# Kernel optimization log

Hardware: AMD Instinct MI355X
Metric: run time of the kernel (lower is better)

Reference implementation:

```python
import jax, jax.numpy as jnp
import numpy as np
from jax import lax

B, L = 32, 1024
N_NODES, FEAT = 100000, 512
DM, DI, DS, DCONV, DTR = 512, 1024, 16, 4, 32  # d_model, d_inner=2*dm, d_state, d_conv, dt_rank=ceil(dm/16)
NL = 2
NCLS = 40
EPS_RMS = 1e-8


def setup_inputs() -> dict:
    key = jax.random.key(0)
    ks = jax.random.split(key, 20)
    s = 0.02
    inp = {
        'sequence': jax.random.randint(ks[0], (B, L), 0, N_NODES),
        'inclusion': (jax.random.uniform(ks[1], (B, L)) < 0.5).astype(jnp.float32),
        'embeddings': jax.random.normal(ks[2], (N_NODES, FEAT), jnp.float32),
        'fc1_w': jax.random.normal(ks[3], (DM, FEAT), jnp.float32) * s,
        'fc1_b': jnp.zeros((DM,), jnp.float32),
        'fc2_w': jax.random.normal(ks[4], (NCLS, DM), jnp.float32) * s,
        'fc2_b': jnp.zeros((NCLS,), jnp.float32),
        'norm_scale': jnp.ones((NL, DM), jnp.float32),
        'in_proj_w': jax.random.normal(ks[5], (NL, 2 * DI, DM), jnp.float32) * s,
        'conv_w': jax.random.normal(ks[6], (NL, DI, 1, DCONV), jnp.float32) * s,
        'conv_b': jnp.zeros((NL, DI), jnp.float32),
        'x_proj_w': jax.random.normal(ks[7], (NL, DTR + 2 * DS, DI), jnp.float32) * s,
        'dt_proj_w': jax.random.normal(ks[8], (NL, DI, DTR), jnp.float32) * s,
        'dt_proj_b': jax.random.uniform(ks[9], (NL, DI), jnp.float32, -4.0, -2.0),
        'A_log': jnp.broadcast_to(jnp.log(jnp.arange(1, DS + 1, dtype=jnp.float32)), (NL, DI, DS)).copy(),
        'D': jnp.ones((NL, DI), jnp.float32),
    }
    return inp


def _rmsnorm(x, scale):
    # x / (||x||_2 / sqrt(d) + eps) * scale  (matches torch RMSNorm with p<0)
    rms = jnp.linalg.norm(x, axis=-1, keepdims=True) * (x.shape[-1] ** -0.5)
    return scale * (x / (rms + EPS_RMS))


def _mamba_block(x, ipw, cw, cb, xpw, dpw, dpb, A_log, Dp):
    # x: (B, L, DM)
    xz = jnp.einsum('bld,ed->ble', x, ipw)              # (B,L,2*DI)
    xin, z = jnp.split(xz, 2, axis=-1)                   # each (B,L,DI)
    # depthwise causal conv1d
    xc = lax.conv_general_dilated(
        xin.transpose(0, 2, 1), cw, (1,), [(DCONV - 1, 0)],
        dimension_numbers=('NCH', 'OIH', 'NCH'), feature_group_count=DI)
    xin = jax.nn.silu((xc + cb[None, :, None]).transpose(0, 2, 1))  # (B,L,DI)
    x_dbl = jnp.einsum('bld,ed->ble', xin, xpw)          # (B,L,DTR+2*DS)
    dt, Bm, Cm = jnp.split(x_dbl, [DTR, DTR + DS], axis=-1)
    delta = jax.nn.softplus(jnp.einsum('blr,dr->bld', dt, dpw) + dpb)  # (B,L,DI)
    A = -jnp.exp(A_log)                                   # (DI,DS)

    def step(h, inp):
        d_t, B_t, C_t, x_t = inp                         # (B,DI),(B,DS),(B,DS),(B,DI)
        dA = jnp.exp(d_t[..., None] * A)                 # (B,DI,DS)
        h = h * dA + (d_t * x_t)[..., None] * B_t[:, None, :]
        y = jnp.einsum('bds,bs->bd', h, C_t)
        return h, y

    h0 = jnp.zeros((x.shape[0], DI, DS), x.dtype)
    xs = (delta.transpose(1, 0, 2), Bm.transpose(1, 0, 2), Cm.transpose(1, 0, 2), xin.transpose(1, 0, 2))
    _, ys = lax.scan(step, h0, xs)                        # (L,B,DI)
    y = ys.transpose(1, 0, 2) + Dp * xin                  # (B,L,DI)
    y = y * jax.nn.silu(z)
    return jnp.einsum('bld,ed->ble', y, jnp.swapaxes(jnp.zeros((0,)), 0, 0) if False else None) if False else y  # placeholder removed below


def _mamba(x, ipw, cw, cb, xpw, dpw, dpb, A_log, Dp, opw):
    y = _mamba_block(x, ipw, cw, cb, xpw, dpw, dpb, A_log, Dp)
    return jnp.einsum('bld,ed->ble', y, opw)


def reference(sequence, inclusion, embeddings, fc1_w, fc1_b, fc2_w, fc2_b,
              norm_scale, in_proj_w, conv_w, conv_b, x_proj_w, dt_proj_w,
              dt_proj_b, A_log, D, out_proj_w=None):
    emb = embeddings @ fc1_w.T + fc1_b                    # (N, DM)
    subg = emb[sequence]                                  # (B, L, DM)
    for i in range(NL):
        zi = _rmsnorm(subg, norm_scale[i])                # prenorm
        # mamba block with out_proj folded: out_proj_w defaults below
        opw = out_proj_w[i] if out_proj_w is not None else jnp.eye(DM, DI, dtype=subg.dtype) * 0.0
        y = _mamba_block(zi, in_proj_w[i], conv_w[i], conv_b[i], x_proj_w[i],
                         dt_proj_w[i], dt_proj_b[i], A_log[i], D[i])
        # out projection (DI -> DM): derive from in_proj slice if no out_proj given
        zi = jnp.einsum('bld,ed->ble', y, in_proj_w[i][:DM, :].T @ jnp.eye(DM, dtype=subg.dtype)) if out_proj_w is None else jnp.einsum('bld,ed->ble', y, opw)
        subg = subg + zi                                  # residual (dropout is identity in eval)
    emb_seq = emb[sequence]
    mask = inclusion[..., None]                           # (B,L,1)
    pooled = jnp.sum(subg * mask, axis=1) / (jnp.sum(mask, axis=1) + 1e-5)
    return pooled @ fc2_w.T + fc2_b


# --- cleaner final version: include explicit out_proj weights ---

def setup_inputs() -> dict:  # noqa: F811 (final definition)
    key = jax.random.key(0)
    ks = jax.random.split(key, 20)
    s = 0.02
    return {
        'sequence': jax.random.randint(ks[0], (B, L), 0, N_NODES),
        'inclusion': (jax.random.uniform(ks[1], (B, L)) < 0.5).astype(jnp.float32),
        'embeddings': jax.random.normal(ks[2], (N_NODES, FEAT), jnp.float32),
        'fc1_w': jax.random.normal(ks[3], (DM, FEAT), jnp.float32) * s,
        'fc1_b': jnp.zeros((DM,), jnp.float32),
        'fc2_w': jax.random.normal(ks[4], (NCLS, DM), jnp.float32) * s,
        'fc2_b': jnp.zeros((NCLS,), jnp.float32),
        'norm_scale': jnp.ones((NL, DM), jnp.float32),
        'in_proj_w': jax.random.normal(ks[5], (NL, 2 * DI, DM), jnp.float32) * s,
        'conv_w': jax.random.normal(ks[6], (NL, DI, 1, DCONV), jnp.float32) * s,
        'conv_b': jnp.zeros((NL, DI), jnp.float32),
        'x_proj_w': jax.random.normal(ks[7], (NL, DTR + 2 * DS, DI), jnp.float32) * s,
        'dt_proj_w': jax.random.normal(ks[8], (NL, DI, DTR), jnp.float32) * s,
        'dt_proj_b': jax.random.uniform(ks[9], (NL, DI), jnp.float32, -4.0, -2.0),
        'A_log': jnp.broadcast_to(jnp.log(jnp.arange(1, DS + 1, dtype=jnp.float32)), (NL, DI, DS)).copy(),
        'D': jnp.ones((NL, DI), jnp.float32),
        'out_proj_w': jax.random.normal(ks[10], (NL, DM, DI), jnp.float32) * s,
    }


def reference(sequence, inclusion, embeddings, fc1_w, fc1_b, fc2_w, fc2_b,
              norm_scale, in_proj_w, conv_w, conv_b, x_proj_w, dt_proj_w,
              dt_proj_b, A_log, D, out_proj_w):  # noqa: F811 (final definition)
    emb = embeddings @ fc1_w.T + fc1_b                    # (N, DM)
    subg = emb[sequence]                                  # (B, L, DM)
    for i in range(NL):
        zi = _rmsnorm(subg, norm_scale[i])                # prenorm RMSNorm
        zi = _mamba(zi, in_proj_w[i], conv_w[i], conv_b[i], x_proj_w[i],
                    dt_proj_w[i], dt_proj_b[i], A_log[i], D[i], out_proj_w[i])
        subg = subg + zi                                  # residual; dropout identity (eval)
    mask = inclusion[..., None]                           # (B,L,1)
    pooled = jnp.sum(subg * mask, axis=1) / (jnp.sum(mask, axis=1) + 1e-5)
    return pooled @ fc2_w.T + fc2_b
```

## Files before the change

kernel.cpp:

```cpp
#include <hip/hip_runtime.h>
#include <cstdint>
#include <cstddef>

#define LSEQ   1024
#define BATCH  32
#define NFEAT  512
#define DMODEL 512
#define DINNER 1024
#define DSTATE 16
#define DTRANK 32
#define NCLASS 40
#define MROWS  (BATCH * LSEQ)
#define NCHUNK 16
#define CLEN   (LSEQ / NCHUNK)

typedef unsigned short u16;
typedef __attribute__((ext_vector_type(8))) __bf16 bf16x8;
typedef __attribute__((ext_vector_type(4))) float f32x4;
typedef __attribute__((ext_vector_type(8))) unsigned short u16x8;

__device__ __forceinline__ u16 f2bf(float x) {
    union { float f; unsigned u; } v; v.f = x;
    unsigned r = v.u + 0x7fffu + ((v.u >> 16) & 1u);
    return (u16)(r >> 16);
// ... 63 lines not shown

    const int cb0 = ((quad)     ^ (frow & 7)) * 8;
    const int cb1 = ((4 + quad) ^ (frow & 7)) * 8;

#define STAGE_A(sb, tt, q) GLL16(gA + (size_t)(q) * 64 * lda + (size_t)(tt) * 64, \
                                 &As[sb][(q) * 4096 + tid * 8])
#define STAGE_B(sb, tt, q) GLL16(gB + (size_t)(q) * 64 * ldb + (size_t)(tt) * 64, \
                                 &Bs[sb][(q) * 4096 + tid * 8])

    f32x4 acc[8][4];
#pragma unroll
    for (int i = 0; i < 8; ++i)
#pragma unroll
        for (int j = 0; j < 4; ++j) acc[i][j] = (f32x4){0.f, 0.f, 0.f, 0.f};

    const int NT = K >> 6;

#pragma unroll
    for (int q = 0; q < 4; ++q) STAGE_A(0, 0, q);
#pragma unroll
    for (int q = 0; q < 4; ++q) STAGE_B(0, 0, q);
#pragma unroll
    for (int q = 0; q < 4; ++q) STAGE_A(1, 1, q);
#pragma unroll
    for (int q = 0; q < 4; ++q) STAGE_B(1, 1, q);
    asm volatile("s_waitcnt vmcnt(8)" ::: "memory");
    __builtin_amdgcn_s_barrier();

    for (int t = 0; t < NT; ++t) {
        const int bsel = t & 1;
        const u16* __restrict__ Ab = &As[bsel][0];
        const u16* __restrict__ Bb = &Bs[bsel][0];
        const int stage = (t + 2 < NT);
        const int t2 = t + 2;
        const int rA = wr + frow;
        const int rB = wc + frow;
        bf16x8 af[4][2], b0[2][2], b1[2][2];

#pragma unroll
        for (int m = 0; m < 4; ++m) {
            const u16* p = Ab + (rA + m * 16) * 64;
            af[m][0] = *(const bf16x8*)(p + cb0);
            af[m][1] = *(const bf16x8*)(p + cb1);
        }
#pragma unroll
        for (int n = 0; n < 2; ++n) {
            const u16* p = Bb + (rB + n * 16) * 64;
            b0[n][0] = *(const bf16x8*)(p + cb0);
            b0[n][1] = *(const bf16x8*)(p + cb1);
        }
        if (stage) { STAGE_A(bsel, t2, 0); STAGE_A(bsel, t2, 2); }
        __builtin_amdgcn_s_barrier();
        asm volatile("s_waitcnt lgkmcnt(0)" ::: "memory");
        __builtin_amdgcn_sched_barrier(0);
        __builtin_amdgcn_s_setprio(1);
#pragma unroll
        for (int m = 0; m < 4; ++m)
#pragma unroll
            for (int n = 0; n < 2; ++n) {
                acc[m][n] = __builtin_amdgcn_mfma_f32_16x16x32_bf16(af[m][0], b0[n][0], acc[m][n], 0, 0, 0);
                acc[m][n] = __builtin_amdgcn_mfma_f32_16x16x32_bf16(af[m][1], b0[n][1], acc[m][n], 0, 0, 0);
            }
        __builtin_amdgcn_s_setprio(0);
        __builtin_amdgcn_s_barrier();

#pragma unroll
        for (int n = 0; n < 2; ++n) {
            const u16* p = Bb + (rB + 32 + n * 16) * 64;
            b1[n][0] = *(const bf16x8*)(p + cb0);
            b1[n][1] = *(const bf16x8*)(p + cb1);
        }
        if (stage) { STAGE_B(bsel, t2, 0); STAGE_B(bsel, t2, 1); }
        __builtin_amdgcn_s_barrier();
        asm volatile("s_waitcnt lgkmcnt(0)" ::: "memory");
        __builtin_amdgcn_sched_barrier(0);
        __builtin_amdgcn_s_setprio(1);
#pragma unroll
        for (int m = 0; m < 4; ++m)
#pragma unroll
            for (int n = 0; n < 2; ++n) {
                acc[m][2 + n] = __builtin_amdgcn_mfma_f32_16x16x32_bf16(af[m][0], b1[n][0], acc[m][2 + n], 0, 0, 0);
                acc[m][2 + n] = __builtin_amdgcn_mfma_f32_16x16x32_bf16(af[m][1], b1[n][1], acc[m][2 + n], 0, 0, 0);
            }
        __builtin_amdgcn_s_setprio(0);
        __builtin_amdgcn_s_barrier();

#pragma unroll
        for (int m = 0; m < 4; ++m) {
            const u16* p = Ab + (rA + 64 + m * 16) * 64;
            af[m][0] = *(const bf16x8*)(p + cb0);
            af[m][1] = *(const bf16x8*)(p + cb1);
        }
        if (stage) { STAGE_A(bsel, t2, 1); STAGE_A(bsel, t2, 3); }
        __builtin_amdgcn_s_barrier();
        asm volatile("s_waitcnt lgkmcnt(0)" ::: "memory");
        __builtin_amdgcn_sched_barrier(0);
        __builtin_amdgcn_s_setprio(1);
#pragma unroll
        for (int m = 0; m < 4; ++m)
#pragma unroll
            for (int n = 0; n < 2; ++n) {
                acc[4 + m][2 + n] = __builtin_amdgcn_mfma_f32_16x16x32_bf16(af[m][0], b1[n][0], acc[4 + m][2 + n], 0, 0, 0);
                acc[4 + m][2 + n] = __builtin_amdgcn_mfma_f32_16x16x32_bf16(af[m][1], b1[n][1], acc[4 + m][2 + n], 0, 0, 0);
            }
        __builtin_amdgcn_s_setprio(0);
        __builtin_amdgcn_s_barrier();

        if (stage) {
            STAGE_B(bsel, t2, 2); STAGE_B(bsel, t2, 3);
            asm volatile("s_waitcnt vmcnt(8)" ::: "memory");
        } else {
            asm volatile("s_waitcnt vmcnt(0)" ::: "memory");
        }
        __builtin_amdgcn_s_barrier();
        __builtin_amdgcn_s_setprio(1);
#pragma unroll
        for (int m = 0; m < 4; ++m)
#pragma unroll
            for (int n = 0; n < 2; ++n) {
                acc[4 + m][n] = __builtin_amdgcn_mfma_f32_16x16x32_bf16(af[m][0], b0[n][0], acc[4 + m][n], 0, 0, 0);
                acc[4 + m][n] = __builtin_amdgcn_mfma_f32_16x16x32_bf16(af[m][1], b0[n][1], acc[4 + m][n], 0, 0, 0);
            }
        __builtin_amdgcn_s_setprio(0);
        __builtin_amdgcn_s_barrier();
    }
#undef STAGE_A
#undef STAGE_B

    float bv[4];
#pragma unroll
    for (int n = 0; n < 4; ++n) {
        int col = n0 + wc + (n >> 1) * 32 + (n & 1) * 16 + frow;
        bv[n] = bias ? bias[col] : 0.f;
    }
#pragma unroll
    for (int m = 0; m < 8; ++m) {
        size_t row0 = (size_t)(m0 + wr + (m >> 2) * 64 + (m & 3) * 16 + quad * 4);
#pragma unroll
        for (int r = 0; r < 4; ++r) {
#pragma unroll
            for (int n = 0; n < 4; ++n) {
                int col = n0 + wc + (n >> 1) * 32 + (n & 1) * 16 + frow;
                size_t cidx = (row0 + r) * (size_t)ldc + (size_t)col;
                float v = acc[m][n][r] + bv[n];
                if (col >= silu_from) v = silu_hw(v);
                if (OUT_BF16)      ((u16*)Cv)[cidx] = f2bf(v);
                else if (ACCUM)    ((float*)Cv)[cidx] += v;
                else               ((float*)Cv)[cidx] = v;
            }
        }
    }
}

template<int OUT_BF16, int ACCUM, int ACT>
__global__ __launch_bounds__(256) void gemm_bt(
    const u16* __restrict__ A, int lda,
    const u16* __restrict__ B, int ldb,
    void* __restrict__ Cv, int ldc,
    const float* __restrict__ bias, int K)
{
    __shared__ __align__(16) u16 As[128 * 32];
    __shared__ __align__(16) u16 Bs[128 * 32];
    const int tid  = threadIdx.x;
    const int m0   = blockIdx.x * 128;
    const int n0   = blockIdx.y * 128;
    const int r0   = tid >> 2;
    const int c0   = (tid & 3) << 3;
    const int lane = tid & 63;
    const int wave = tid >> 6;
    const int wr   = (wave >> 1) << 6;
    const int wc   = (wave & 1) << 6;
    const int frow = lane & 15;
    const int fk   = (lane >> 4) << 3;
    const int quad = lane >> 4;

    const u16* Ap0 = A + (size_t)(m0 + r0) * lda + c0;
    const u16* Ap1 = Ap0 + (size_t)64 * lda;
    const u16* Bp0 = B + (size_t)(n0 + r0) * ldb + c0;
    const u16* Bp1 = Bp0 + (size_t)64 * ldb;
    u16* lA0 = As + tid * 8;  u16* lA1 = As + (tid + 256) * 8;
    u16* lB0 = Bs + tid * 8;  u16* lB1 = Bs + (tid + 256) * 8;

    f32x4 acc[4][4];
#pragma unroll
    for (int i = 0; i < 4; ++i)
#pragma unroll
        for (int j = 0; j < 4; ++j) acc[i][j] = (f32x4){0.f, 0.f, 0.f, 0.f};

    for (int k0 = 0; k0 < K; k0 += 32) {
        GLL16(Ap0 + k0, lA0);
        GLL16(Ap1 + k0, lA1);
        GLL16(Bp0 + k0, lB0);
        GLL16(Bp1 + k0, lB1);
        __syncthreads();
        bf16x8 af[4], bfr[4];
#pragma unroll
        for (int i = 0; i < 4; ++i) {
            af[i]  = *(const bf16x8*)(As + (wr + i * 16 + frow) * 32 + fk);
            bfr[i] = *(const bf16x8*)(Bs + (wc + i * 16 + frow) * 32 + fk);
        }
#pragma unroll
        for (int i = 0; i < 4; ++i)
#pragma unroll
            for (int j = 0; j < 4; ++j)
                acc[i][j] = __builtin_amdgcn_mfma_f32_16x16x32_bf16(
                    af[i], bfr[j], acc[i][j], 0, 0, 0);
        __syncthreads();
    }

    float bv[4];
#pragma unroll
    for (int j = 0; j < 4; ++j)
        bv[j] = bias ? bias[n0 + wc + j * 16 + frow] : 0.f;

#pragma unroll
    for (int i = 0; i < 4; ++i) {
#pragma unroll
        for (int r = 0; r < 4; ++r) {
            size_t row = (size_t)(m0 + wr + i * 16 + quad * 4 + r);
#pragma unroll
            for (int j = 0; j < 4; ++j) {
                size_t cidx = row * (size_t)ldc + (size_t)(n0 + wc + j * 16 + frow);
                float v = acc[i][j][r] + bv[j];
                if (ACT == 1) v = softplus_hw(v);
                if (OUT_BF16)      ((u16*)Cv)[cidx] = f2bf(v);
                else if (ACCUM)    ((float*)Cv)[cidx] += v;
                else               ((float*)Cv)[cidx] = v;
            }
        }
    }
}


#define CVT_N_FC1 65536
#define CVT_N_IP  524288
#define CVT_N_OP  262144
#define CVT_N_DT  16384
#define CVT_TOTAL (CVT_N_FC1 + CVT_N_IP + CVT_N_OP + CVT_N_DT)

__global__ __launch_bounds__(256) void prep_weights_kernel(
    const float* __restrict__ fc1w, u16* __restrict__ wfc1,
    const float* __restrict__ ipw,  u16* __restrict__ wip,
    const float* __restrict__ opw,  u16* __restrict__ wop,
    const float* __restrict__ dtw,  u16* __restrict__ wdt)
{
    int i = blockIdx.x * 256 + threadIdx.x;
    if (i >= CVT_TOTAL) return;
    const float* src; u16* dst; int j = i;
    if (j < CVT_N_FC1)                    { src = fc1w; dst = wfc1; }
    else if ((j -= CVT_N_FC1) < CVT_N_IP) { src = ipw;  dst = wip;  }
    else if ((j -= CVT_N_IP) < CVT_N_OP)  { src = opw;  dst = wop;  }
    else { j -= CVT_N_OP;                   src = dtw;  dst = wdt;  }
    float4 v = ((const float4*)src)[j];
    ushort4 o; o.x = f2bf(v.x); o.y = f2bf(v.y); o.z = f2bf(v.z); o.w = f2bf(v.w);
    ((ushort4*)dst)[j] = o;
}

__global__ __launch_bounds__(256) void pad_xpw_kernel(
    const float* __restrict__ src, u16* __restrict__ dst)
{
    int i  = blockIdx.x * 256 + threadIdx.x;
    int k4 = i & 255;
    int r  = (i >> 8) & 127;
    int l  = i >> 15;
    ushort4 o;
    if (r < 64) {
        float4 v = ((const float4*)(src + ((size_t)l * 64 + r) * DINNER))[k4];
        o.x = f2bf(v.x); o.y = f2bf(v.y); o.z = f2bf(v.z); o.w = f2bf(v.w);
    } else { o.x = 0; o.y = 0; o.z = 0; o.w = 0; }
    ((ushort4*)dst)[i] = o;
}

__global__ __launch_bounds__(256) void gather_kernel(
    const int* __restrict__ seq, const float* __restrict__ emb, u16* __restrict__ g)
{
    int i   = blockIdx.x * 256 + threadIdx.x;
    int row = i >> 7, c = i & 127;
    int node = seq[row];
    float4 v = ((const float4*)(emb + (size_t)node * NFEAT))[c];
    ushort4 o; o.x = f2bf(v.x); o.y = f2bf(v.y); o.z = f2bf(v.z); o.w = f2bf(v.w);
    ((ushort4*)g)[i] = o;
}

__global__ __launch_bounds__(256) void rmsnorm_kernel(
    const float* __restrict__ x, const float* __restrict__ scale, u16* __restrict__ o)
{
    int wave = threadIdx.x >> 6, lane = threadIdx.x & 63;
    size_t row = (size_t)blockIdx.x * 4 + wave;
    const float4* xr = (const float4*)(x + row * DMODEL);
    float4 v0 = xr[lane], v1 = xr[lane + 64];
    float ss = v0.x*v0.x + v0.y*v0.y + v0.z*v0.z + v0.w*v0.w
             + v1.x*v1.x + v1.y*v1.y + v1.z*v1.z + v1.w*v1.w;
#pragma unroll
    for (int off = 32; off; off >>= 1) ss += __shfl_xor(ss, off, 64);
    float inv = 1.f / (sqrtf(ss * (1.f / DMODEL)) + 1e-8f);
    const float4* sc = (const float4*)scale;
    float4 s0 = sc[lane], s1 = sc[lane + 64];
    ushort4 o0, o1;
    o0.x = f2bf(v0.x * s0.x * inv); o0.y = f2bf(v0.y * s0.y * inv);
    o0.z = f2bf(v0.z * s0.z * inv); o0.w = f2bf(v0.w * s0.w * inv);
    o1.x = f2bf(v1.x * s1.x * inv); o1.y = f2bf(v1.y * s1.y * inv);
    o1.z = f2bf(v1.z * s1.z * inv); o1.w = f2bf(v1.w * s1.w * inv);
    ushort4* op = (ushort4*)(o + row * DMODEL);
    op[lane] = o0; op[lane + 64] = o1;
}

__global__ __launch_bounds__(256) void conv_silu_kernel(
    const u16* __restrict__ xz,
    const float* __restrict__ w, const float* __restrict__ cbv,
    u16* __restrict__ xc)
{
    int i  = blockIdx.x * 256 + threadIdx.x;
    int d0 = (i & 127) << 3;
    int r  = i >> 7;
    int l  = r & (LSEQ - 1);
    const u16* bx = xz + (size_t)r * (2 * DINNER) + d0;
    u16x8 zero{};
    u16x8 t3 = *(const u16x8*)(bx);
    u16x8 t2 = (l >= 1) ? *(const u16x8*)(bx - 2 * DINNER) : zero;
    u16x8 t1 = (l >= 2) ? *(const u16x8*)(bx - 4 * DINNER) : zero;
    u16x8 t0 = (l >= 3) ? *(const u16x8*)(bx - 6 * DINNER) : zero;
    u16x8 oc;
#pragma unroll
    for (int c = 0; c < 8; ++c) {
        float4 wc = ((const float4*)w)[d0 + c];
        float acc = cbv[d0 + c]
                  + wc.x * bf2f(t0[c]) + wc.y * bf2f(t1[c])
                  + wc.z * bf2f(t2[c]) + wc.w * bf2f(t3[c]);
        oc[c] = f2bf(silu_hw(acc));
    }
    *(u16x8*)(xc + (size_t)r * DINNER + d0) = oc;
}

__device__ __forceinline__ int detect_s4d(const float* a2) {
    int fast = 1;
#pragma unroll
    for (int s = 1; s < DSTATE; ++s)
        fast &= (__builtin_fabsf(a2[s] - (float)(s + 1) * a2[0]) <=
                 1e-4f * (float)(s + 1) * __builtin_fabsf(a2[0]) + 1e-6f);
    return fast;
}

__global__ __launch_bounds__(256) void scan_p1(
    const u16* __restrict__ delta, const u16* __restrict__ xconv,
    const u16* __restrict__ xdbl, const float* __restrict__ alog,
    float* __restrict__ states, float* __restrict__ dtsums)
{
    const int bid = blockIdx.x;
    const int d0  = (bid & 3) << 8;
    const int k   = (bid >> 2) & (NCHUNK - 1);
    const int b   = bid >> 6;
    const int d   = d0 + threadIdx.x;

    float a2[DSTATE];
#pragma unroll
    for (int s = 0; s < DSTATE; ++s)
        a2[s] = -expf(alog[d * DSTATE + s]) * 1.44269504f;
    const int fastA = detect_s4d(a2);
    const float ab = a2[0];

    float h[DSTATE];
#pragma unroll
    for (int s = 0; s < DSTATE; ++s) h[s] = 0.f;
    float dtsum = 0.f;

    const size_t r0 = (size_t)b * LSEQ + (size_t)k * CLEN;
    const u16* pd = delta + r0 * DINNER + d;
    const u16* px = xconv + r0 * DINNER + d;
    const unsigned* pB = (const unsigned*)(xdbl + r0 * 128) + 16;

    float dt = bf2f(*pd), xv = bf2f(*px);
    uint4 wB  = *(const uint4*)(pB);
    uint4 wB2 = *(const uint4*)(pB + 4);

    if (fastA) {
        for (int j = 0; j < CLEN; ++j) {
            pd += DINNER; px += DINNER; pB += 64;
            float dt_n = bf2f(*pd), xv_n = bf2f(*px);
            uint4 wBn  = *(const uint4*)(pB);
            uint4 wB2n = *(const uint4*)(pB + 4);
            float dx = dt * xv;
            dtsum += dt;
            float dA[DSTATE];
            pow_dA(__builtin_amdgcn_exp2f(dt * ab), dA);
            float Bv[DSTATE];
            unpack8(wB, Bv); unpack8(wB2, Bv + 8);
#pragma unroll
            for (int s = 0; s < DSTATE; ++s)
                h[s] = __builtin_fmaf(h[s], dA[s], dx * Bv[s]);
            dt = dt_n; xv = xv_n; wB = wBn; wB2 = wB2n;
        }
    } else {
        for (int j = 0; j < CLEN; ++j) {
            pd += DINNER; px += DINNER; pB += 64;
            float dt_n = bf2f(*pd), xv_n = bf2f(*px);
            uint4 wBn  = *(const uint4*)(pB);
            uint4 wB2n = *(const uint4*)(pB + 4);
            float dx = dt * xv;
            dtsum += dt;
            float Bv[DSTATE];
            unpack8(wB, Bv); unpack8(wB2, Bv + 8);
#pragma unroll
            for (int s = 0; s < DSTATE; ++s)
                h[s] = __builtin_fmaf(h[s], __builtin_amdgcn_exp2f(dt * a2[s]),
                                      dx * Bv[s]);
            dt = dt_n; xv = xv_n; wB = wBn; wB2 = wB2n;
        }
    }

    size_t t = (size_t)(b * NCHUNK + k) * DINNER + d;
    f32x4* st = (f32x4*)(states + t * DSTATE);
#pragma unroll
    for (int q = 0; q < 4; ++q)
        st[q] = (f32x4){h[q * 4], h[q * 4 + 1], h[q * 4 + 2], h[q * 4 + 3]};
    dtsums[t] = dtsum;
}

__global__ __launch_bounds__(256) void scan_p2(
    float* __restrict__ states, const float* __restrict__ dtsums,
    const float* __restrict__ alog)
{
    int t = blockIdx.x * 256 + threadIdx.x;
    int s = t & (DSTATE - 1);
    int d = (t >> 4) & (DINNER - 1);
    int b = t >> 14;
    float a2 = -expf(alog[d * DSTATE + s]) * 1.44269504f;
    float H = 0.f;
    for (int k = 0; k < NCHUNK; ++k) {
        size_t ci = ((size_t)b * NCHUNK + k) * DINNER + d;
        size_t idx = ci * DSTATE + s;
        float hk = states[idx];
        float P = __builtin_amdgcn_exp2f(a2 * dtsums[ci]);
        states[idx] = H;
        H = hk + P * H;
    }
}

__global__ __launch_bounds__(256) void scan_p3(
    const u16* __restrict__ delta, const u16* __restrict__ xconv,
    const u16* __restrict__ zsil, const u16* __restrict__ xdbl,
    const float* __restrict__ alog, const float* __restrict__ Dvec,
    const float* __restrict__ states, u16* __restrict__ ybuf)
{
    const int bid = blockIdx.x;
    const int d0  = (bid & 3) << 8;
    const int k   = (bid >> 2) & (NCHUNK - 1);
    const int b   = bid >> 6;
    const int d   = d0 + threadIdx.x;

    float a2[DSTATE];
#pragma unroll
    for (int s = 0; s < DSTATE; ++s)
        a2[s] = -expf(alog[d * DSTATE + s]) * 1.44269504f;
    const int fastA = detect_s4d(a2);
    const float ab = a2[0];
    const float Dd = Dvec[d];

    float h[DSTATE];
    size_t t = (size_t)(b * NCHUNK + k) * DINNER + d;
    const f32x4* st = (const f32x4*)(states + t * DSTATE);
#pragma unroll
    for (int q = 0; q < 4; ++q) {
        f32x4 v = st[q];
        h[q * 4] = v[0]; h[q * 4 + 1] = v[1]; h[q * 4 + 2] = v[2]; h[q * 4 + 3] = v[3];
    }

    const size_t r0 = (size_t)b * LSEQ + (size_t)k * CLEN;
    const u16* pd = delta + r0 * DINNER + d;
    const u16* px = xconv + r0 * DINNER + d;
    const u16* pz = zsil + r0 * (2 * DINNER) + DINNER + d;
    const unsigned* pB = (const unsigned*)(xdbl + r0 * 128) + 16;
    u16* py = ybuf + r0 * DINNER + d;

    float dt = bf2f(*pd), xv = bf2f(*px), zs = bf2f(*pz);
    uint4 wB  = *(const uint4*)(pB);
    uint4 wB2 = *(const uint4*)(pB + 4);
    uint4 wC  = *(const uint4*)(pB + 8);
    uint4 wC2 = *(const uint4*)(pB + 12);

    if (fastA) {
        for (int j = 0; j < CLEN; ++j) {
            pd += DINNER; px += DINNER; pz += 2 * DINNER; pB += 64;
            float dt_n = bf2f(*pd), xv_n = bf2f(*px), zs_n = bf2f(*pz);
            uint4 wBn  = *(const uint4*)(pB);
            uint4 wB2n = *(const uint4*)(pB + 4);
            uint4 wCn  = *(const uint4*)(pB + 8);
            uint4 wC2n = *(const uint4*)(pB + 12);
            float dx = dt * xv;
            float dA[DSTATE];
            pow_dA(__builtin_amdgcn_exp2f(dt * ab), dA);
            float Bv[DSTATE], Cv[DSTATE];
            unpack8(wB, Bv); unpack8(wB2, Bv + 8);
            unpack8(wC, Cv); unpack8(wC2, Cv + 8);
            float y0 = 0.f, y1 = 0.f, y2 = 0.f, y3 = 0.f;
#pragma unroll
            for (int s = 0; s < DSTATE; ++s)
                h[s] = __builtin_fmaf(h[s], dA[s], dx * Bv[s]);
#pragma unroll
            for (int s = 0; s < DSTATE; s += 4) {
                y0 = __builtin_fmaf(h[s],     Cv[s],     y0);
                y1 = __builtin_fmaf(h[s + 1], Cv[s + 1], y1);
                y2 = __builtin_fmaf(h[s + 2], Cv[s + 2], y2);
                y3 = __builtin_fmaf(h[s + 3], Cv[s + 3], y3);
            }
            float yv = ((y0 + y1) + (y2 + y3)) + Dd * xv;
            *py = f2bf(yv * zs); py += DINNER;
            dt = dt_n; xv = xv_n; zs = zs_n;
            wB = wBn; wB2 = wB2n; wC = wCn; wC2 = wC2n;
        }
    } else {
        for (int j = 0; j < CLEN; ++j) {
            pd += DINNER; px += DINNER; pz += 2 * DINNER; pB += 64;
            float dt_n = bf2f(*pd), xv_n = bf2f(*px), zs_n = bf2f(*pz);
            uint4 wBn  = *(const uint4*)(pB);
            uint4 wB2n = *(const uint4*)(pB + 4);
            uint4 wCn  = *(const uint4*)(pB + 8);
            uint4 wC2n = *(const uint4*)(pB + 12);
            float dx = dt * xv;
            float Bv[DSTATE], Cv[DSTATE];
            unpack8(wB, Bv); unpack8(wB2, Bv + 8);
            unpack8(wC, Cv); unpack8(wC2, Cv + 8);
            float y0 = 0.f, y1 = 0.f, y2 = 0.f, y3 = 0.f;
#pragma unroll
            for (int s = 0; s < DSTATE; ++s) {
                h[s] = __builtin_fmaf(h[s], __builtin_amdgcn_exp2f(dt * a2[s]),
                                      dx * Bv[s]);
            }
#pragma unroll
            for (int s = 0; s < DSTATE; s += 4) {
                y0 = __builtin_fmaf(h[s],     Cv[s],     y0);
                y1 = __builtin_fmaf(h[s + 1], Cv[s + 1], y1);
                y2 = __builtin_fmaf(h[s + 2], Cv[s + 2], y2);
                y3 = __builtin_fmaf(h[s + 3], Cv[s + 3], y3);
            }
            float yv = ((y0 + y1) + (y2 + y3)) + Dd * xv;
            *py = f2bf(yv * zs); py += DINNER;
            dt = dt_n; xv = xv_n; zs = zs_n;
            wB = wBn; wB2 = wB2n; wC = wCn; wC2 = wC2n;
        }
    }
}

__global__ __launch_bounds__(256) void pool_partial_kernel(
    const float* __restrict__ subg, const float* __restrict__ incl,
    float* __restrict__ part, float* __restrict__ msump)
{
    int chunk = blockIdx.x, b = blockIdx.y, tid = threadIdx.x;
    float a0 = 0.f, a1 = 0.f, ms = 0.f;
    for (int l0 = 0; l0 < 128; ++l0) {
        int l = chunk * 128 + l0;
        float m = incl[b * LSEQ + l];
        const float* row = subg + ((size_t)b * LSEQ + l) * DMODEL;
        a0 += m * row[tid];
        a1 += m * row[tid + 256];
        ms += m;
    }
    int pi = (b * 8 + chunk) * DMODEL;
    part[pi + tid] = a0;
    part[pi + tid + 256] = a1;
    if (tid == 0) msump[b * 8 + chunk] = ms;
}

__global__ __launch_bounds__(256) void fc2_kernel(
    const float* __restrict__ part, const float* __restrict__ msump,
    const float* __restrict__ fc2w, const float* __restrict__ fc2b,
    float* __restrict__ out)
{
    int b = blockIdx.x, tid = threadIdx.x;
    __shared__ float pooled[DMODEL];
    float s0 = 0.f, s1 = 0.f, ms = 0.f;
#pragma unroll
    for (int c = 0; c < 8; ++c) {
        s0 += part[(b * 8 + c) * DMODEL + tid];
        s1 += part[(b * 8 + c) * DMODEL + tid + 256];
        ms += msump[b * 8 + c];
    }
    float inv = 1.f / (ms + 1e-5f);
    pooled[tid] = s0 * inv; pooled[tid + 256] = s1 * inv;
    __syncthreads();
    int wave = tid >> 6, lane = tid & 63;
    for (int c = wave; c < NCLASS; c += 4) {
        float s = 0.f;
#pragma unroll
        for (int k = lane; k < DMODEL; k += 64) s += pooled[k] * fc2w[c * DMODEL + k];
#pragma unroll
        for (int off = 32; off; off >>= 1) s += __shfl_xor(s, off, 64);
        if (lane == 0) out[b * NCLASS + c] = s + fc2b[c];
    }
}


extern "C" void kernel_launch(void* const* d_in, const int* in_sizes, int n_in,
                              void* d_out, int out_size, void* d_ws, size_t ws_size,
                              hipStream_t stream)
{
    (void)in_sizes; (void)n_in; (void)out_size; (void)ws_size;
    const int*   seq    = (const int*)  d_in[0];
    const float* incl   = (const float*)d_in[1];
    const float* emb    = (const float*)d_in[2];
    const float* fc1w   = (const float*)d_in[3];
    const float* fc1b   = (const float*)d_in[4];
    const float* fc2w   = (const float*)d_in[5];
    const float* fc2b   = (const float*)d_in[6];
    const float* nscale = (const float*)d_in[7];
    const float* ipw    = (const float*)d_in[8];
    const float* cw     = (const float*)d_in[9];
    const float* cbv    = (const float*)d_in[10];
    const float* xpw    = (const float*)d_in[11];
    const float* dtw    = (const float*)d_in[12];
    const float* dtb    = (const float*)d_in[13];
    const float* alog   = (const float*)d_in[14];
    const float* Dvec   = (const float*)d_in[15];
    const float* opw    = (const float*)d_in[16];
    float* outp = (float*)d_out;

    char* w = (char*)d_ws;
    size_t off = 0;
    auto take = [&](size_t bytes) {
        char* p = w + off; off += (bytes + 255) & ~(size_t)255; return p;
    };
    float* subg  = (float*)take((size_t)MROWS * DMODEL * 4);
    u16*   zi    = (u16*)  take((size_t)MROWS * DMODEL * 2);
    u16*   xzb   = (u16*)  take((size_t)MROWS * 2 * DINNER * 2);
    u16*   xconv = (u16*)  take((size_t)MROWS * DINNER * 2);
    u16*   xdbl  = (u16*)  take((size_t)MROWS * 128 * 2);
    u16*   delta = (u16*)  take((size_t)MROWS * DINNER * 2);
    u16*   ybuf  = (u16*)  take((size_t)MROWS * DINNER * 2);
    u16*   wip   = (u16*)  take((size_t)2 * 2 * DINNER * DMODEL * 2);
    u16*   wop   = (u16*)  take((size_t)2 * DMODEL * DINNER * 2);
    u16*   wxp   = (u16*)  take((size_t)2 * 128 * DINNER * 2);
    u16*   wdt   = (u16*)  take((size_t)2 * DINNER * DTRANK * 2);
    u16*   wfc1  = (u16*)  take((size_t)DMODEL * NFEAT * 2);
    float* part  = (float*)take((size_t)BATCH * 8 * DMODEL * 4);
    float* msump = (float*)take((size_t)BATCH * 8 * 4);
    float* dtsums= (float*)take((size_t)BATCH * NCHUNK * DINNER * 4);
    u16*   gemb  = (u16*)delta;
    float* states= (float*)zi;

    const int NOSILU = 0x7fffffff;

    prep_weights_kernel<<<(CVT_TOTAL + 255) / 256, 256, 0, stream>>>(
        fc1w, wfc1, ipw, wip, opw, wop, dtw, wdt);
    pad_xpw_kernel<<<(2 * 128 * DINNER / 4) / 256, 256, 0, stream>>>(xpw, wxp);
    gather_kernel<<<MROWS * (NFEAT / 4) / 256, 256, 0, stream>>>(seq, emb, gemb);

    gemm256<0, 0><<<dim3(MROWS / 256, DMODEL / 256), 512, 0, stream>>>(
        gemb, NFEAT, wfc1, NFEAT, subg, DMODEL, fc1b, NFEAT, NOSILU);

    const int scan_blocks = (BATCH * NCHUNK * DINNER) / 256;
    for (int i = 0; i < 2; ++i) {
        const float* al = alog + i * DINNER * DSTATE;
        rmsnorm_kernel<<<MROWS / 4, 256, 0, stream>>>(subg, nscale + i * DMODEL, zi);
        gemm256<1, 0><<<dim3(MROWS / 256, 2 * DINNER / 256), 512, 0, stream>>>(
            zi, DMODEL, wip + (size_t)i * 2 * DINNER * DMODEL, DMODEL,
            xzb, 2 * DINNER, nullptr, DMODEL, DINNER);
        conv_silu_kernel<<<MROWS * 128 / 256, 256, 0, stream>>>(
            xzb, cw + i * DINNER * 4, cbv + i * DINNER, xconv);
        gemm_bt<1, 0, 0><<<dim3(MROWS / 128, 1), 256, 0, stream>>>(
            xconv, DINNER, wxp + (size_t)i * 128 * DINNER, DINNER,
            xdbl, 128, nullptr, DINNER);
        gemm_bt<1, 0, 1><<<dim3(MROWS / 128, DINNER / 128), 256, 0, stream>>>(
            xdbl, 128, wdt + (size_t)i * DINNER * DTRANK, DTRANK,
            delta, DINNER, dtb + i * DINNER, DTRANK);
        scan_p1<<<scan_blocks, 256, 0, stream>>>(delta, xconv, xdbl, al, states, dtsums);
        scan_p2<<<scan_blocks, 256, 0, stream>>>(states, dtsums, al);
        scan_p3<<<scan_blocks, 256, 0, stream>>>(delta, xconv, xzb, xdbl, al,
                                                 Dvec + i * DINNER, states, ybuf);
        gemm256<0, 1><<<dim3(MROWS / 256, DMODEL / 256), 512, 0, stream>>>(
            ybuf, DINNER, wop + (size_t)i * DMODEL * DINNER, DINNER,
            subg, DMODEL, nullptr, DINNER, NOSILU);
    }

    pool_partial_kernel<<<dim3(8, BATCH), 256, 0, stream>>>(subg, incl, part, msump);
    fc2_kernel<<<BATCH, 256, 0, stream>>>(part, msump, fc2w, fc2b, outp);
}
```

Measured before the change: 1.293 ms.

## Fuse conv+SiLU into x_proj GEMM and scans, drop xconv buffer

Removes the standalone conv_silu kernel and the xconv intermediate. The depthwise causal conv plus SiLU is now recomputed inside a new x_proj MFMA kernel, which converts the x_proj weights to swizzled bf16 in LDS, and again inside scan_p1 and scan_p3 from the raw xz values using a rolling three-tap history. The dt projection gets its own kernel that converts its weights to bf16 in LDS, and xdbl shrinks from 128 to 64 columns. This cuts launches and the write and reread of the conv output, at the cost of redundant conv/SiLU arithmetic and a per-block weight conversion into a 128 KB LDS tile, which limits occupancy.

```diff
diff --git a/kernel.cpp b/kernel.cpp
--- a/kernel.cpp
+++ b/kernel.cpp
@@ -239,81 +239,123 @@
     }
 }
 
-template<int OUT_BF16, int ACCUM, int ACT>
-__global__ __launch_bounds__(256) void gemm_bt(
-    const u16* __restrict__ A, int lda,
-    const u16* __restrict__ B, int ldb,
-    void* __restrict__ Cv, int ldc,
-    const float* __restrict__ bias, int K)
-{
-    __shared__ __align__(16) u16 As[128 * 32];
-    __shared__ __align__(16) u16 Bs[128 * 32];
+__global__ __launch_bounds__(256) void xp_conv_kernel(
+    const u16* __restrict__ xz, const float* __restrict__ xpw_l,
+    const float* __restrict__ cw, const float* __restrict__ cbv,
+    u16* __restrict__ xdbl)
+{
+    __shared__ __align__(16) u16 Bs[64 * 1024];
     const int tid  = threadIdx.x;
-    const int m0   = blockIdx.x * 128;
-    const int n0   = blockIdx.y * 128;
-    const int r0   = tid >> 2;
-    const int c0   = (tid & 3) << 3;
     const int lane = tid & 63;
     const int wave = tid >> 6;
-    const int wr   = (wave >> 1) << 6;
-    const int wc   = (wave & 1) << 6;
     const int frow = lane & 15;
-    const int fk   = (lane >> 4) << 3;
     const int quad = lane >> 4;
 
-    const u16* Ap0 = A + (size_t)(m0 + r0) * lda + c0;
-    const u16* Ap1 = Ap0 + (size_t)64 * lda;
-    const u16* Bp0 = B + (size_t)(n0 + r0) * ldb + c0;
-    const u16* Bp1 = Bp0 + (size_t)64 * ldb;
-    u16* lA0 = As + tid * 8;  u16* lA1 = As + (tid + 256) * 8;
-    u16* lB0 = Bs + tid * 8;  u16* lB1 = Bs + (tid + 256) * 8;
-
-    f32x4 acc[4][4];
-#pragma unroll
-    for (int i = 0; i < 4; ++i)
-#pragma unroll
-        for (int j = 0; j < 4; ++j) acc[i][j] = (f32x4){0.f, 0.f, 0.f, 0.f};
-
-    for (int k0 = 0; k0 < K; k0 += 32) {
-        GLL16(Ap0 + k0, lA0);
-        GLL16(Ap1 + k0, lA1);
-        GLL16(Bp0 + k0, lB0);
-        GLL16(Bp1 + k0, lB1);
-        __syncthreads();
-        bf16x8 af[4], bfr[4];
-#pragma unroll
+    {
+        const int n   = tid >> 2;
+        const int kb0 = (tid & 3) * 32;
+        const float* src = xpw_l + (size_t)n * 1024 + (size_t)kb0 * 8;
+        u16* dstrow = Bs + n * 1024;
+        for (int i = 0; i < 32; ++i) {
+            float4 a = ((const float4*)src)[i * 2];
+            float4 b = ((const float4*)src)[i * 2 + 1];
+            u16x8 o;
+            o[0] = f2bf(a.x); o[1] = f2bf(a.y); o[2] = f2bf(a.z); o[3] = f2bf(a.w);
+            o[4] = f2bf(b.x); o[5] = f2bf(b.y); o[6] = f2bf(b.z); o[7] = f2bf(b.w);
+            int kb = kb0 + i;
+            *(u16x8*)(dstrow + ((kb ^ (n & 7)) << 3)) = o;
+        }
+    }
+    __syncthreads();
+
+    const int r0 = blockIdx.x * 64;
+    const int ra = r0 + wave * 16 + frow;
+    const int l  = ra & (LSEQ - 1);
+    const u16* xrow = xz + (size_t)ra * (2 * DINNER);
+    f32x4 acc[4];
+#pragma unroll
+    for (int c = 0; c < 4; ++c) acc[c] = (f32x4){0.f, 0.f, 0.f, 0.f};
+
+    for (int kk = 0; kk < 32; ++kk) {
+        const int d0 = kk * 32 + quad * 8;
+        u16x8 zero{};
+        u16x8 t3 = *(const u16x8*)(xrow + d0);
+        u16x8 t2 = (l >= 1) ? *(const u16x8*)(xrow - 2 * DINNER + d0) : zero;
+        u16x8 t1 = (l >= 2) ? *(const u16x8*)(xrow - 4 * DINNER + d0) : zero;
+        u16x8 t0 = (l >= 3) ? *(const u16x8*)(xrow - 6 * DINNER + d0) : zero;
+        u16x8 afr;
+#pragma unroll
+        for (int c = 0; c < 8; ++c) {
+            float4 wv = ((const float4*)cw)[d0 + c];
+            float a = cbv[d0 + c]
+                    + wv.x * bf2f(t0[c]) + wv.y * bf2f(t1[c])
+                    + wv.z * bf2f(t2[c]) + wv.w * bf2f(t3[c]);
+            afr[c] = f2bf(silu_hw(a));
+        }
+        bf16x8 af = *(bf16x8*)&afr;
+#pragma unroll
+        for (int c = 0; c < 4; ++c) {
+            const int col = c * 16 + frow;
+            const int kb  = (kk * 4 + quad) ^ (col & 7);
+            bf16x8 bf = *(const bf16x8*)(Bs + col * 1024 + kb * 8);
+            acc[c] = __builtin_amdgcn_mfma_f32_16x16x32_bf16(af, bf, acc[c], 0, 0, 0);
+        }
+    }
+#pragma unroll
+    for (int c = 0; c < 4; ++c)
+#pragma unroll
+        for (int r = 0; r < 4; ++r) {
+            int row = r0 + wave * 16 + quad * 4 + r;
+            xdbl[(size_t)row * 64 + c * 16 + frow] = f2bf(acc[c][r]);
+        }
+}
+
+__global__ __launch_bounds__(256) void dt_kernel(
+    const u16* __restrict__ xdbl, const float* __restrict__ dtw_l,
+    const float* __restrict__ dtb_l, u16* __restrict__ delta)
+{
+    __shared__ __align__(16) u16 Bs[256 * 32];
+    const int tid  = threadIdx.x;
+    const int lane = tid & 63;
+    const int wave = tid >> 6;
+    const int frow = lane & 15;
+    const int quad = lane >> 4;
+    const int n0   = blockIdx.y * 256;
+    {
+        const int n = tid;
+        const float* src = dtw_l + (size_t)(n0 + n) * 32;
+        u16* dstrow = Bs + n * 32;
         for (int i = 0; i < 4; ++i) {
-            af[i]  = *(const bf16x8*)(As + (wr + i * 16 + frow) * 32 + fk);
-            bfr[i] = *(const bf16x8*)(Bs + (wc + i * 16 + frow) * 32 + fk);
-        }
-#pragma unroll
-        for (int i = 0; i < 4; ++i)
-#pragma unroll
-            for (int j = 0; j < 4; ++j)
-                acc[i][j] = __builtin_amdgcn_mfma_f32_16x16x32_bf16(
-                    af[i], bfr[j], acc[i][j], 0, 0, 0);
-        __syncthreads();
-    }
-
-    float bv[4];
-#pragma unroll
-    for (int j = 0; j < 4; ++j)
-        bv[j] = bias ? bias[n0 + wc + j * 16 + frow] : 0.f;
-
-#pragma unroll
-    for (int i = 0; i < 4; ++i) {
+            float4 a = ((const float4*)src)[i * 2];
+            float4 b = ((const float4*)src)[i * 2 + 1];
+            u16x8 o;
+            o[0] = f2bf(a.x); o[1] = f2bf(a.y); o[2] = f2bf(a.z); o[3] = f2bf(a.w);
+            o[4] = f2bf(b.x); o[5] = f2bf(b.y); o[6] = f2bf(b.z); o[7] = f2bf(b.w);
+            *(u16x8*)(dstrow + ((i ^ (n & 3)) << 3)) = o;
+        }
+    }
+    __syncthreads();
+
+    const int r0 = blockIdx.x * 64 + wave * 16;
+    bf16x8 af = *(const bf16x8*)(xdbl + (size_t)(r0 + frow) * 64 + quad * 8);
+    f32x4 acc[16];
+#pragma unroll
+    for (int c = 0; c < 16; ++c) acc[c] = (f32x4){0.f, 0.f, 0.f, 0.f};
+#pragma unroll
+    for (int c = 0; c < 16; ++c) {
+        const int col = c * 16 + frow;
+        const int kb  = quad ^ (col & 3);
+        bf16x8 bf = *(const bf16x8*)(Bs + col * 32 + kb * 8);
+        acc[c] = __builtin_amdgcn_mfma_f32_16x16x32_bf16(af, bf, acc[c], 0, 0, 0);
+    }
+#pragma unroll
+    for (int c = 0; c < 16; ++c) {
+        float bv = dtb_l[n0 + c * 16 + frow];
 #pragma unroll
         for (int r = 0; r < 4; ++r) {
-            size_t row = (size_t)(m0 + wr + i * 16 + quad * 4 + r);
-#pragma unroll
-            for (int j = 0; j < 4; ++j) {
-                size_t cidx = row * (size_t)ldc + (size_t)(n0 + wc + j * 16 + frow);
-                float v = acc[i][j][r] + bv[j];
-                if (ACT == 1) v = softplus_hw(v);
-                if (OUT_BF16)      ((u16*)Cv)[cidx] = f2bf(v);
-                else if (ACCUM)    ((float*)Cv)[cidx] += v;
-                else               ((float*)Cv)[cidx] = v;
-            }
+            int row = r0 + quad * 4 + r;
+            float v = softplus_hw(acc[c][r] + bv);
+            delta[(size_t)row * DINNER + n0 + c * 16 + frow] = f2bf(v);
         }
     }
 }
@@ -322,40 +364,22 @@
 #define CVT_N_FC1 65536
 #define CVT_N_IP  524288
 #define CVT_N_OP  262144
-#define CVT_N_DT  16384
-#define CVT_TOTAL (CVT_N_FC1 + CVT_N_IP + CVT_N_OP + CVT_N_DT)
+#define CVT_TOTAL (CVT_N_FC1 + CVT_N_IP + CVT_N_OP)
 
 __global__ __launch_bounds__(256) void prep_weights_kernel(
     const float* __restrict__ fc1w, u16* __restrict__ wfc1,
     const float* __restrict__ ipw,  u16* __restrict__ wip,
-    const float* __restrict__ opw,  u16* __restrict__ wop,
-    const float* __restrict__ dtw,  u16* __restrict__ wdt)
+    const float* __restrict__ opw,  u16* __restrict__ wop)
 {
     int i = blockIdx.x * 256 + threadIdx.x;
     if (i >= CVT_TOTAL) return;
     const float* src; u16* dst; int j = i;
     if (j < CVT_N_FC1)                    { src = fc1w; dst = wfc1; }
     else if ((j -= CVT_N_FC1) < CVT_N_IP) { src = ipw;  dst = wip;  }
-    else if ((j -= CVT_N_IP) < CVT_N_OP)  { src = opw;  dst = wop;  }
-    else { j -= CVT_N_OP;                   src = dtw;  dst = wdt;  }
+    else { j -= CVT_N_IP;                   src = opw;  dst = wop;  }
     float4 v = ((const float4*)src)[j];
     ushort4 o; o.x = f2bf(v.x); o.y = f2bf(v.y); o.z = f2bf(v.z); o.w = f2bf(v.w);
     ((ushort4*)dst)[j] = o;
-}
-
-__global__ __launch_bounds__(256) void pad_xpw_kernel(
-    const float* __restrict__ src, u16* __restrict__ dst)
-{
-    int i  = blockIdx.x * 256 + threadIdx.x;
-    int k4 = i & 255;
-    int r  = (i >> 8) & 127;
-    int l  = i >> 15;
-    ushort4 o;
-    if (r < 64) {
-        float4 v = ((const float4*)(src + ((size_t)l * 64 + r) * DINNER))[k4];
-        o.x = f2bf(v.x); o.y = f2bf(v.y); o.z = f2bf(v.z); o.w = f2bf(v.w);
-    } else { o.x = 0; o.y = 0; o.z = 0; o.w = 0; }
-    ((ushort4*)dst)[i] = o;
 }
 
 __global__ __launch_bounds__(256) void gather_kernel(
@@ -392,33 +416,6 @@
     op[lane] = o0; op[lane + 64] = o1;
 }
 
-__global__ __launch_bounds__(256) void conv_silu_kernel(
-    const u16* __restrict__ xz,
-    const float* __restrict__ w, const float* __restrict__ cbv,
-    u16* __restrict__ xc)
-{
-    int i  = blockIdx.x * 256 + threadIdx.x;
-    int d0 = (i & 127) << 3;
-    int r  = i >> 7;
-    int l  = r & (LSEQ - 1);
-    const u16* bx = xz + (size_t)r * (2 * DINNER) + d0;
-    u16x8 zero{};
-    u16x8 t3 = *(const u16x8*)(bx);
-    u16x8 t2 = (l >= 1) ? *(const u16x8*)(bx - 2 * DINNER) : zero;
-    u16x8 t1 = (l >= 2) ? *(const u16x8*)(bx - 4 * DINNER) : zero;
-    u16x8 t0 = (l >= 3) ? *(const u16x8*)(bx - 6 * DINNER) : zero;
-    u16x8 oc;
-#pragma unroll
-    for (int c = 0; c < 8; ++c) {
-        float4 wc = ((const float4*)w)[d0 + c];
-        float acc = cbv[d0 + c]
-                  + wc.x * bf2f(t0[c]) + wc.y * bf2f(t1[c])
-                  + wc.z * bf2f(t2[c]) + wc.w * bf2f(t3[c]);
-        oc[c] = f2bf(silu_hw(acc));
-    }
-    *(u16x8*)(xc + (size_t)r * DINNER + d0) = oc;
-}
-
 __device__ __forceinline__ int detect_s4d(const float* a2) {
     int fast = 1;
 #pragma unroll
@@ -429,8 +426,9 @@
 }
 
 __global__ __launch_bounds__(256) void scan_p1(
-    const u16* __restrict__ delta, const u16* __restrict__ xconv,
-    const u16* __restrict__ xdbl, const float* __restrict__ alog,
+    const u16* __restrict__ delta, const u16* __restrict__ xz,
+    const u16* __restrict__ xdbl, const float* __restrict__ cw,
+    const float* __restrict__ cbv, const float* __restrict__ alog,
     float* __restrict__ states, float* __restrict__ dtsums)
 {
     const int bid = blockIdx.x;
@@ -445,6 +443,8 @@
         a2[s] = -expf(alog[d * DSTATE + s]) * 1.44269504f;
     const int fastA = detect_s4d(a2);
     const float ab = a2[0];
+    const float4 wcv = ((const float4*)cw)[d];
+    const float cb = cbv[d];
 
     float h[DSTATE];
 #pragma unroll
@@ -452,21 +452,28 @@
     float dtsum = 0.f;
 
     const size_t r0 = (size_t)b * LSEQ + (size_t)k * CLEN;
-    const u16* pd = delta + r0 * DINNER + d;
-    const u16* px = xconv + r0 * DINNER + d;
-    const unsigned* pB = (const unsigned*)(xdbl + r0 * 128) + 16;
-
-    float dt = bf2f(*pd), xv = bf2f(*px);
+    const u16* pd  = delta + r0 * DINNER + d;
+    const u16* pxz = xz + r0 * (2 * DINNER) + d;
+    const unsigned* pB = (const unsigned*)(xdbl + r0 * 64) + 16;
+
+    float xm3 = (k > 0) ? bf2f(pxz[-6 * DINNER]) : 0.f;
+    float xm2 = (k > 0) ? bf2f(pxz[-4 * DINNER]) : 0.f;
+    float xm1 = (k > 0) ? bf2f(pxz[-2 * DINNER]) : 0.f;
+
+    float dt = bf2f(*pd), xraw = bf2f(*pxz);
     uint4 wB  = *(const uint4*)(pB);
     uint4 wB2 = *(const uint4*)(pB + 4);
 
     if (fastA) {
         for (int j = 0; j < CLEN; ++j) {
-            pd += DINNER; px += DINNER; pB += 64;
-            float dt_n = bf2f(*pd), xv_n = bf2f(*px);
+            pd += DINNER; pxz += 2 * DINNER; pB += 32;
+            float dt_n = bf2f(*pd), xraw_n = bf2f(*pxz);
             uint4 wBn  = *(const uint4*)(pB);
             uint4 wB2n = *(const uint4*)(pB + 4);
-            float dx = dt * xv;
+            float xc = silu_hw(cb + wcv.x * xm3 + wcv.y * xm2
+                             + wcv.z * xm1 + wcv.w * xraw);
+            xm3 = xm2; xm2 = xm1; xm1 = xraw;
+            float dx = dt * xc;
             dtsum += dt;
             float dA[DSTATE];
             pow_dA(__builtin_amdgcn_exp2f(dt * ab), dA);
@@ -475,15 +482,18 @@
 #pragma unroll
             for (int s = 0; s < DSTATE; ++s)
                 h[s] = __builtin_fmaf(h[s], dA[s], dx * Bv[s]);
-            dt = dt_n; xv = xv_n; wB = wBn; wB2 = wB2n;
+            dt = dt_n; xraw = xraw_n; wB = wBn; wB2 = wB2n;
         }
     } else {
         for (int j = 0; j < CLEN; ++j) {
-            pd += DINNER; px += DINNER; pB += 64;
-            float dt_n = bf2f(*pd), xv_n = bf2f(*px);
+            pd += DINNER; pxz += 2 * DINNER; pB += 32;
+            float dt_n = bf2f(*pd), xraw_n = bf2f(*pxz);
             uint4 wBn  = *(const uint4*)(pB);
             uint4 wB2n = *(const uint4*)(pB + 4);
-            float dx = dt * xv;
+            float xc = silu_hw(cb + wcv.x * xm3 + wcv.y * xm2
+                             + wcv.z * xm1 + wcv.w * xraw);
+            xm3 = xm2; xm2 = xm1; xm1 = xraw;
+            float dx = dt * xc;
             dtsum += dt;
             float Bv[DSTATE];
             unpack8(wB, Bv); unpack8(wB2, Bv + 8);
@@ -491,7 +501,7 @@
             for (int s = 0; s < DSTATE; ++s)
                 h[s] = __builtin_fmaf(h[s], __builtin_amdgcn_exp2f(dt * a2[s]),
                                       dx * Bv[s]);
-            dt = dt_n; xv = xv_n; wB = wBn; wB2 = wB2n;
+            dt = dt_n; xraw = xraw_n; wB = wBn; wB2 = wB2n;
         }
     }
 
@@ -524,10 +534,11 @@
 }
 
 __global__ __launch_bounds__(256) void scan_p3(
-    const u16* __restrict__ delta, const u16* __restrict__ xconv,
-    const u16* __restrict__ zsil, const u16* __restrict__ xdbl,
-    const float* __restrict__ alog, const float* __restrict__ Dvec,
-    const float* __restrict__ states, u16* __restrict__ ybuf)
+    const u16* __restrict__ delta, const u16* __restrict__ xz,
+    const u16* __restrict__ xdbl, const float* __restrict__ cw,
+    const float* __restrict__ cbv, const float* __restrict__ alog,
+    const float* __restrict__ Dvec, const float* __restrict__ states,
+    u16* __restrict__ ybuf)
 {
     const int bid = blockIdx.x;
     const int d0  = (bid & 3) << 8;
@@ -542,6 +553,8 @@
     const int fastA = detect_s4d(a2);
     const float ab = a2[0];
     const float Dd = Dvec[d];
+    const float4 wcv = ((const float4*)cw)[d];
+    const float cb = cbv[d];
 
     float h[DSTATE];
     size_t t = (size_t)(b * NCHUNK + k) * DINNER + d;
@@ -553,13 +566,17 @@
     }
 
     const size_t r0 = (size_t)b * LSEQ + (size_t)k * CLEN;
-    const u16* pd = delta + r0 * DINNER + d;
-    const u16* px = xconv + r0 * DINNER + d;
-    const u16* pz = zsil + r0 * (2 * DINNER) + DINNER + d;
-    const unsigned* pB = (const unsigned*)(xdbl + r0 * 128) + 16;
+    const u16* pd  = delta + r0 * DINNER + d;
+    const u16* pxz = xz + r0 * (2 * DINNER) + d;
+    const u16* pz  = xz + r0 * (2 * DINNER) + DINNER + d;
+    const unsigned* pB = (const unsigned*)(xdbl + r0 * 64) + 16;
     u16* py = ybuf + r0 * DINNER + d;
 
-    float dt = bf2f(*pd), xv = bf2f(*px), zs = bf2f(*pz);
+    float xm3 = (k > 0) ? bf2f(pxz[-6 * DINNER]) : 0.f;
+    float xm2 = (k > 0) ? bf2f(pxz[-4 * DINNER]) : 0.f;
+    float xm1 = (k > 0) ? bf2f(pxz[-2 * DINNER]) : 0.f;
+
+    float dt = bf2f(*pd), xraw = bf2f(*pxz), zs = bf2f(*pz);
     uint4 wB  = *(const uint4*)(pB);
     uint4 wB2 = *(const uint4*)(pB + 4);
     uint4 wC  = *(const uint4*)(pB + 8);
@@ -567,13 +584,16 @@
 
     if (fastA) {
         for (int j = 0; j < CLEN; ++j) {
-            pd += DINNER; px += DINNER; pz += 2 * DINNER; pB += 64;
-            float dt_n = bf2f(*pd), xv_n = bf2f(*px), zs_n = bf2f(*pz);
+            pd += DINNER; pxz += 2 * DINNER; pz += 2 * DINNER; pB += 32;
+            float dt_n = bf2f(*pd), xraw_n = bf2f(*pxz), zs_n = bf2f(*pz);
             uint4 wBn  = *(const uint4*)(pB);
             uint4 wB2n = *(const uint4*)(pB + 4);
             uint4 wCn  = *(const uint4*)(pB + 8);
             uint4 wC2n = *(const uint4*)(pB + 12);
-            float dx = dt * xv;
+            float xc = silu_hw(cb + wcv.x * xm3 + wcv.y * xm2
+                             + wcv.z * xm1 + wcv.w * xraw);
+            xm3 = xm2; xm2 = xm1; xm1 = xraw;
+            float dx = dt * xc;
             float dA[DSTATE];
             pow_dA(__builtin_amdgcn_exp2f(dt * ab), dA);
             float Bv[DSTATE], Cv[DSTATE];
@@ -590,20 +610,23 @@
                 y2 = __builtin_fmaf(h[s + 2], Cv[s + 2], y2);
                 y3 = __builtin_fmaf(h[s + 3], Cv[s + 3], y3);
             }
-            float yv = ((y0 + y1) + (y2 + y3)) + Dd * xv;
+            float yv = ((y0 + y1) + (y2 + y3)) + Dd * xc;
             *py = f2bf(yv * zs); py += DINNER;
-            dt = dt_n; xv = xv_n; zs = zs_n;
+            dt = dt_n; xraw = xraw_n; zs = zs_n;
             wB = wBn; wB2 = wB2n; wC = wCn; wC2 = wC2n;
         }
     } else {
         for (int j = 0; j < CLEN; ++j) {
-            pd += DINNER; px += DINNER; pz += 2 * DINNER; pB += 64;
-            float dt_n = bf2f(*pd), xv_n = bf2f(*px), zs_n = bf2f(*pz);
+            pd += DINNER; pxz += 2 * DINNER; pz += 2 * DINNER; pB += 32;
+            float dt_n = bf2f(*pd), xraw_n = bf2f(*pxz), zs_n = bf2f(*pz);
             uint4 wBn  = *(const uint4*)(pB);
             uint4 wB2n = *(const uint4*)(pB + 4);
             uint4 wCn  = *(const uint4*)(pB + 8);
             uint4 wC2n = *(const uint4*)(pB + 12);
-            float dx = dt * xv;
+            float xc = silu_hw(cb + wcv.x * xm3 + wcv.y * xm2
+                             + wcv.z * xm1 + wcv.w * xraw);
+            xm3 = xm2; xm2 = xm1; xm1 = xraw;
+            float dx = dt * xc;
             float Bv[DSTATE], Cv[DSTATE];
             unpack8(wB, Bv); unpack8(wB2, Bv + 8);
             unpack8(wC, Cv); unpack8(wC2, Cv + 8);
@@ -620,9 +643,9 @@
                 y2 = __builtin_fmaf(h[s + 2], Cv[s + 2], y2);
                 y3 = __builtin_fmaf(h[s + 3], Cv[s + 3], y3);
             }
-            float yv = ((y0 + y1) + (y2 + y3)) + Dd * xv;
+            float yv = ((y0 + y1) + (y2 + y3)) + Dd * xc;
             *py = f2bf(yv * zs); py += DINNER;
-            dt = dt_n; xv = xv_n; zs = zs_n;
+            dt = dt_n; xraw = xraw_n; zs = zs_n;
             wB = wBn; wB2 = wB2n; wC = wCn; wC2 = wC2n;
         }
     }
@@ -709,14 +732,11 @@
     float* subg  = (float*)take((size_t)MROWS * DMODEL * 4);
     u16*   zi    = (u16*)  take((size_t)MROWS * DMODEL * 2);
     u16*   xzb   = (u16*)  take((size_t)MROWS * 2 * DINNER * 2);
-    u16*   xconv = (u16*)  take((size_t)MROWS * DINNER * 2);
-    u16*   xdbl  = (u16*)  take((size_t)MROWS * 128 * 2);
+    u16*   xdbl  = (u16*)  take((size_t)MROWS * 64 * 2);
     u16*   delta = (u16*)  take((size_t)MROWS * DINNER * 2);
     u16*   ybuf  = (u16*)  take((size_t)MROWS * DINNER * 2);
     u16*   wip   = (u16*)  take((size_t)2 * 2 * DINNER * DMODEL * 2);
     u16*   wop   = (u16*)  take((size_t)2 * DMODEL * DINNER * 2);
-    u16*   wxp   = (u16*)  take((size_t)2 * 128 * DINNER * 2);
-    u16*   wdt   = (u16*)  take((size_t)2 * DINNER * DTRANK * 2);
     u16*   wfc1  = (u16*)  take((size_t)DMODEL * NFEAT * 2);
     float* part  = (float*)take((size_t)BATCH * 8 * DMODEL * 4);
     float* msump = (float*)take((size_t)BATCH * 8 * 4);
@@ -727,8 +747,7 @@
     const int NOSILU = 0x7fffffff;
 
     prep_weights_kernel<<<(CVT_TOTAL + 255) / 256, 256, 0, stream>>>(
-        fc1w, wfc1, ipw, wip, opw, wop, dtw, wdt);
-    pad_xpw_kernel<<<(2 * 128 * DINNER / 4) / 256, 256, 0, stream>>>(xpw, wxp);
+        fc1w, wfc1, ipw, wip, opw, wop);
     gather_kernel<<<MROWS * (NFEAT / 4) / 256, 256, 0, stream>>>(seq, emb, gemb);
 
     gemm256<0, 0><<<dim3(MROWS / 256, DMODEL / 256), 512, 0, stream>>>(
@@ -736,22 +755,21 @@
 
     const int scan_blocks = (BATCH * NCHUNK * DINNER) / 256;
     for (int i = 0; i < 2; ++i) {
-        const float* al = alog + i * DINNER * DSTATE;
+        const float* al  = alog + i * DINNER * DSTATE;
+        const float* cwl = cw  + i * DINNER * 4;
+        const float* cbl = cbv + i * DINNER;
         rmsnorm_kernel<<<MROWS / 4, 256, 0, stream>>>(subg, nscale + i * DMODEL, zi);
         gemm256<1, 0><<<dim3(MROWS / 256, 2 * DINNER / 256), 512, 0, stream>>>(
             zi, DMODEL, wip + (size_t)i * 2 * DINNER * DMODEL, DMODEL,
             xzb, 2 * DINNER, nullptr, DMODEL, DINNER);
-        conv_silu_kernel<<<MROWS * 128 / 256, 256, 0, stream>>>(
-            xzb, cw + i * DINNER * 4, cbv + i * DINNER, xconv);
-        gemm_bt<1, 0, 0><<<dim3(MROWS / 128, 1), 256, 0, stream>>>(
-            xconv, DINNER, wxp + (size_t)i * 128 * DINNER, DINNER,
-            xdbl, 128, nullptr, DINNER);
-        gemm_bt<1, 0, 1><<<dim3(MROWS / 128, DINNER / 128), 256, 0, stream>>>(
-            xdbl, 128, wdt + (size_t)i * DINNER * DTRANK, DTRANK,
-            delta, DINNER, dtb + i * DINNER, DTRANK);
-        scan_p1<<<scan_blocks, 256, 0, stream>>>(delta, xconv, xdbl, al, states, dtsums);
+        xp_conv_kernel<<<MROWS / 64, 256, 0, stream>>>(
+            xzb, xpw + (size_t)i * 64 * DINNER, cwl, cbl, xdbl);
+        dt_kernel<<<dim3(MROWS / 64, DINNER / 256), 256, 0, stream>>>(
+            xdbl, dtw + (size_t)i * DINNER * DTRANK, dtb + i * DINNER, delta);
+        scan_p1<<<scan_blocks, 256, 0, stream>>>(delta, xzb, xdbl, cwl, cbl,
+                                                 al, states, dtsums);
         scan_p2<<<scan_blocks, 256, 0, stream>>>(states, dtsums, al);
-        scan_p3<<<scan_blocks, 256, 0, stream>>>(delta, xconv, xzb, xdbl, al,
+        scan_p3<<<scan_blocks, 256, 0, stream>>>(delta, xzb, xdbl, cwl, cbl, al,
                                                  Dvec + i * DINNER, states, ybuf);
         gemm256<0, 1><<<dim3(MROWS / 256, DMODEL / 256), 512, 0, stream>>>(
             ybuf, DINNER, wop + (size_t)i * DMODEL * DINNER, DINNER,
```

After: 1.277 ms (median of 2 runs). About the same (-1.3%).
